# Kernel optimization log

Hardware: AMD Instinct MI355X
Metric: run time of the kernel (lower is better)

Reference implementation:

```python
import jax, jax.numpy as jnp
import numpy as np
import math

B, S, D, H = 2, 2048, 1024, 16
DK = D // H


def setup_inputs() -> dict:
    key = jax.random.key(0)
    ks = jax.random.split(key, 8)
    s = 1.0 / math.sqrt(D)
    inp = {
        "query": jax.random.normal(ks[0], (B, S, D), jnp.float32),
        "key": jax.random.normal(ks[1], (B, S, D), jnp.float32),
        "value": jax.random.normal(ks[2], (B, S, D), jnp.float32),
        # causal mask: (1, 1, S, S), 1 where attention allowed
        "mask": jnp.tril(jnp.ones((S, S), jnp.int32))[None, None, :, :],
        "Wq": jax.random.normal(ks[3], (D, D), jnp.float32) * s,
        "Wk": jax.random.normal(ks[4], (D, D), jnp.float32) * s,
        "Wv": jax.random.normal(ks[5], (D, D), jnp.float32) * s,
        "Wo": jax.random.normal(ks[6], (D, D), jnp.float32) * s,
    }
    return inp


def reference(query, key, value, mask, Wq, Wk, Wv, Wo):
    # nn.Linear(bias=False): y = x @ W.T
    def proj_heads(x, W):
        y = jnp.einsum("bsd,ed->bse", x, W)          # (B,S,D)
        return y.reshape(B, -1, H, DK).transpose(0, 2, 1, 3)  # (B,H,S,DK)

    q = proj_heads(query, Wq)
    k = proj_heads(key, Wk)
    v = proj_heads(value, Wv)

    scale = jnp.asarray(math.sqrt(DK), q.dtype)
    scores = jnp.einsum("bhqd,bhkd->bhqk", q, k) / scale  # (B,H,S,S)
    scores = jnp.where(mask == 0, -jnp.inf, scores)
    attn = jax.nn.softmax(scores, axis=-1)
    # dropout p=0.0 (eval): identity
    out = jnp.einsum("bhqk,bhkd->bhqd", attn, v)          # (B,H,S,DK)
    concat = out.transpose(0, 2, 1, 3).reshape(B, -1, D)  # (B,S,D)
    return jnp.einsum("bsd,ed->bse", concat, Wo)
```

## Files before the change

kernel.cpp:

```cpp
#include <hip/hip_runtime.h>
#include <hip/hip_bf16.h>

#define B_ 2
#define S_ 2048
#define D_ 1024
#define H_ 16
#define DK_ 64

typedef __hip_bfloat16 bf16;
typedef __attribute__((ext_vector_type(8))) short bf16x8;
typedef __attribute__((ext_vector_type(4))) short bf16x4;
typedef __attribute__((ext_vector_type(4))) float f32x4;

#define GLDS16(g, l)                                                     \
    __builtin_amdgcn_global_load_lds(                                    \
        (const __attribute__((address_space(1))) void*)(g),              \
        (__attribute__((address_space(3))) void*)(l), 16, 0, 0)

#define MFMA_K32(a, b, c) __builtin_amdgcn_mfma_f32_16x16x32_bf16(a, b, c, 0, 0, 0)
#define MFMA_K16(a, b, c) __builtin_amdgcn_mfma_f32_16x16x16bf16_1k(a, b, c, 0, 0, 0)
#define EXP2F(x) __builtin_amdgcn_exp2f(x)

__global__ __launch_bounds__(256) void cvt_all(
    const float* __restrict__ q, const float* __restrict__ k, const float* __restrict__ v,
    const float* __restrict__ w0, const float* __restrict__ w1,
    const float* __restrict__ w2, const float* __restrict__ w3,
    bf16* __restrict__ oq, bf16* __restrict__ ok, bf16* __restrict__ ov,
    bf16* __restrict__ o0, bf16* __restrict__ o1, bf16* __restrict__ o2,
    bf16* __restrict__ o3) {
    int bid = blockIdx.x;
    const float* src; bf16* dst; int base;
    if      (bid < 2048) { src = q;  dst = oq; base = bid; }
    else if (bid < 4096) { src = k;  dst = ok; base = bid - 2048; }
    else if (bid < 6144) { src = v;  dst = ov; base = bid - 4096; }
    else if (bid < 6656) { src = w0; dst = o0; base = bid - 6144; }
    else if (bid < 7168) { src = w1; dst = o1; base = bid - 6656; }
    else if (bid < 7680) { src = w2; dst = o2; base = bid - 7168; }
    else                 { src = w3; dst = o3; base = bid - 7680; }
    int i = (base * 256 + threadIdx.x) * 8;
    float4 a = *(const float4*)(src + i);
    float4 b = *(const float4*)(src + i + 4);
    __align__(16) bf16 o[8];
    o[0] = __float2bfloat16(a.x); o[1] = __float2bfloat16(a.y);
    o[2] = __float2bfloat16(a.z); o[3] = __float2bfloat16(a.w);
    o[4] = __float2bfloat16(b.x); o[5] = __float2bfloat16(b.y);
    o[6] = __float2bfloat16(b.z); o[7] = __float2bfloat16(b.w);
    *(bf16x8*)(dst + i) = *(const bf16x8*)o;
}

__device__ __forceinline__ void proj_loop32(const bf16* __restrict__ X,
                                            const bf16* __restrict__ W,
                                            int m0, int n0, bf16* As, bf16* Bs,
                                            f32x4 (&acc)[4][4]) {
    const int K = D_;
    const int tid = threadIdx.x;
    const int lane = tid & 63, wave = tid >> 6;
    const int lm = lane & 15, quad = lane >> 4;
    const int wr = wave >> 1, wc = wave & 1;

    auto stage = [&](int t, int bf) {
        int k0 = t * 32;
        bf16* Ab = As + bf * (128 * 32);
        bf16* Bb = Bs + bf * (128 * 32);
#pragma unroll
        for (int i = 0; i < 2; ++i) {
            int s = i * 256 + tid;
            int row = s >> 2, c = (s & 3) ^ (row & 3);
            GLDS16(X + (size_t)(m0 + row) * K + k0 + c * 8, Ab + s * 8);
        }
#pragma unroll
        for (int i = 0; i < 2; ++i) {
            int s = i * 256 + tid;
            int row = s >> 2, c = (s & 3) ^ (row & 3);
            GLDS16(W + (size_t)(n0 + row) * K + k0 + c * 8, Bb + s * 8);
        }
    };

    stage(0, 0);
    for (int t = 0; t < K / 32; ++t) {
        __syncthreads();
        if (t + 1 < K / 32) stage(t + 1, (t + 1) & 1);
        const bf16* Ab = As + (t & 1) * (128 * 32);
        const bf16* Bb = Bs + (t & 1) * (128 * 32);
        bf16x8 aF[4], bF[4];
#pragma unroll
        for (int mt = 0; mt < 4; ++mt) {
            int row = wr * 64 + mt * 16 + lm;
            aF[mt] = *(const bf16x8*)(Ab + row * 32 + ((quad ^ (row & 3)) * 8));
        }
#pragma unroll
        for (int nt = 0; nt < 4; ++nt) {
            int row = wc * 64 + nt * 16 + lm;
            bF[nt] = *(const bf16x8*)(Bb + row * 32 + ((quad ^ (row & 3)) * 8));
        }
#pragma unroll
        for (int mt = 0; mt < 4; ++mt)
#pragma unroll
            for (int nt = 0; nt < 4; ++nt)
                acc[mt][nt] = MFMA_K32(aF[mt], bF[nt], acc[mt][nt]);
    }
}

__global__ __launch_bounds__(256) void proj_qkv(
    const bf16* __restrict__ qx, const bf16* __restrict__ kx, const bf16* __restrict__ vx,
    const bf16* __restrict__ wq, const bf16* __restrict__ wk, const bf16* __restrict__ wv,
    bf16* __restrict__ qb, bf16* __restrict__ kb, bf16* __restrict__ vtb) {
    __shared__ __align__(16) bf16 As[2 * 128 * 32];
    __shared__ __align__(16) bf16 Bs[2 * 128 * 32];
    const int L = (int)blockIdx.x;
    const int tile = (L & 7) * 96 + (L >> 3);
    const int z = tile >> 8;
    const int rem = tile & 255;
    const int n0 = (rem & 7) * 128;
    const int m0 = (rem >> 3) * 128;
    const bf16* X = (z == 0) ? qx : (z == 1) ? kx : vx;
    const bf16* W = (z == 0) ? wq : (z == 1) ? wk : wv;
    f32x4 acc[4][4] = {};
    proj_loop32(X, W, m0, n0, As, Bs, acc);

    const int lane = threadIdx.x & 63, wave = threadIdx.x >> 6;
    const int lm = lane & 15, quad = lane >> 4;
    const int wr = wave >> 1, wc = wave & 1;
#pragma unroll
    for (int mt = 0; mt < 4; ++mt) {
        int mbase = m0 + wr * 64 + mt * 16 + quad * 4;
#pragma unroll
        for (int nt = 0; nt < 4; ++nt) {
            int n = n0 + wc * 64 + nt * 16 + lm;
            if (z == 2) {
                int b = mbase >> 11, s = mbase & (S_ - 1);
                unsigned short u[4];
#pragma unroll
                for (int r = 0; r < 4; ++r) {
                    bf16 hv = __float2bfloat16(acc[mt][nt][r]);
                    u[r] = *(unsigned short*)&hv;
                }
                ushort4 pk = {u[0], u[1], u[2], u[3]};
                *(ushort4*)(vtb + ((size_t)(b * 1024 + n) * S_ + s)) = pk;
            } else {
                bf16* Y = z ? kb : qb;
#pragma unroll
                for (int r = 0; r < 4; ++r)
                    Y[(size_t)(mbase + r) * D_ + n] = __float2bfloat16(acc[mt][nt][r]);
            }
        }
    }
}

__global__ __launch_bounds__(256) void proj_o(const bf16* __restrict__ X,
                                              const bf16* __restrict__ W,
                                              float* __restrict__ Y) {
    __shared__ __align__(16) bf16 As[2 * 64 * 32];
    __shared__ __align__(16) bf16 Bs[2 * 128 * 32];
    const int L = (int)blockIdx.x;
    const int tile = (L & 7) * 64 + (L >> 3);
    const int n0 = (tile & 7) * 128;
    const int m0 = (tile >> 3) * 64;

    const int K = D_;
    const int tid = threadIdx.x;
    const int lane = tid & 63, wave = tid >> 6;
    const int lm = lane & 15, quad = lane >> 4;
    const int wr = wave >> 1, wc = wave & 1;

    f32x4 acc[2][4] = {};

    auto stage = [&](int t, int bf) {
        int k0 = t * 32;
        bf16* Ab = As + bf * (64 * 32);
        bf16* Bb = Bs + bf * (128 * 32);
        {
            int s = tid;
            int row = s >> 2, c = (s & 3) ^ (row & 3);
            GLDS16(X + (size_t)(m0 + row) * K + k0 + c * 8, Ab + s * 8);
        }
#pragma unroll
        for (int i = 0; i < 2; ++i) {
            int s = i * 256 + tid;
            int row = s >> 2, c = (s & 3) ^ (row & 3);
            GLDS16(W + (size_t)(n0 + row) * K + k0 + c * 8, Bb + s * 8);
        }
    };

    stage(0, 0);
    for (int t = 0; t < K / 32; ++t) {
        __syncthreads();
        if (t + 1 < K / 32) stage(t + 1, (t + 1) & 1);
        const bf16* Ab = As + (t & 1) * (64 * 32);
        const bf16* Bb = Bs + (t & 1) * (128 * 32);
        bf16x8 aF[2], bF[4];
#pragma unroll
        for (int mt = 0; mt < 2; ++mt) {
            int row = wr * 32 + mt * 16 + lm;
            aF[mt] = *(const bf16x8*)(Ab + row * 32 + ((quad ^ (row & 3)) * 8));
        }
#pragma unroll
        for (int nt = 0; nt < 4; ++nt) {
            int row = wc * 64 + nt * 16 + lm;
            bF[nt] = *(const bf16x8*)(Bb + row * 32 + ((quad ^ (row & 3)) * 8));
        }
#pragma unroll
        for (int mt = 0; mt < 2; ++mt)
#pragma unroll
            for (int nt = 0; nt < 4; ++nt)
                acc[mt][nt] = MFMA_K32(aF[mt], bF[nt], acc[mt][nt]);
    }

#pragma unroll
    for (int mt = 0; mt < 2; ++mt) {
        int mbase = m0 + wr * 32 + mt * 16 + quad * 4;
#pragma unroll
        for (int nt = 0; nt < 4; ++nt) {
            int n = n0 + wc * 64 + nt * 16 + lm;
#pragma unroll
            for (int r = 0; r < 4; ++r)
                Y[(size_t)(mbase + r) * D_ + n] = acc[mt][nt][r];
        }
    }
}

__global__ __launch_bounds__(512) void attn_kernel(const bf16* __restrict__ Q,
                                                   const bf16* __restrict__ Kb,
                                                   const bf16* __restrict__ VT,
                                                   bf16* __restrict__ O) {
    __shared__ __align__(16) bf16 kt[2][128 * 64];
    __shared__ __align__(16) bf16 vt[2][64 * 128];

    const int tid = threadIdx.x;
    const int lane = tid & 63, wave = tid >> 6;
    const int lm = lane & 15, quad = lane >> 4;
    const int f = (int)blockIdx.x;
    const int cls = f & 7;
    const int t = f >> 3;
    const int p = t >> 2;
    const int combo = cls + 8 * (t & 3);
    const int b = combo >> 4, h = combo & 15;
    const int qiA = p, qiB = 15 - p;
    const int q0A = qiA * 128 + wave * 16;
    const int q0B = qiB * 128 + wave * 16;

    const size_t bhoff = (size_t)b * S_ * D_ + (size_t)h * DK_;
    const bf16* vtb = VT + ((size_t)b * 1024 + h * DK_) * S_;

    const bf16* qpA = Q + bhoff + (size_t)(q0A + lm) * D_ + quad * 8;
    bf16x8 aqA0 = *(const bf16x8*)(qpA);
    bf16x8 aqA1 = *(const bf16x8*)(qpA + 32);
    const bf16* qpB = Q + bhoff + (size_t)(q0B + lm) * D_ + quad * 8;
    bf16x8 aqB0 = *(const bf16x8*)(qpB);
    bf16x8 aqB1 = *(const bf16x8*)(qpB + 32);

    f32x4 oaccA[4] = {}, oaccB[4] = {};
    float lsumA = 0.f, lsumB = 0.f;
    const float cexp = 0.125f * 1.44269504f;

    auto stage = [&](int i, int bf) {
        int j0s = i * 128;
#pragma unroll
        for (int ii = 0; ii < 2; ++ii) {
            int s = ii * 512 + tid;
            int j = s >> 3, c = (s & 7) ^ (j & 7);
            GLDS16(Kb + bhoff + (size_t)(j0s + j) * D_ + c * 8, kt[bf] + s * 8);
        }
#pragma unroll
        for (int ii = 0; ii < 2; ++ii) {
            int s = ii * 512 + tid;
            int d = s >> 4, c = (s & 15) ^ (d & 15);
            GLDS16(vtb + (size_t)d * S_ + j0s + c * 8, vt[bf] + s * 8);
        }
    };

    auto chunk = [&](const bf16* ktb, const bf16* vtl, int st, bool mk,
                     bf16x8 aq0, bf16x8 aq1, f32x4 (&oacc)[4], float& lsum) {
        int j = st * 16 + lm;
        bf16x8 bk0 = *(const bf16x8*)(ktb + (((j << 3) | (quad ^ (j & 7))) * 8));
        bf16x8 bk1 = *(const bf16x8*)(ktb + (((j << 3) | ((4 + quad) ^ (j & 7))) * 8));
        f32x4 z = {};
        z = MFMA_K32(bk0, aq0, z);
        z = MFMA_K32(bk1, aq1, z);
        bf16x4 pa;
        float rs = 0.f;
#pragma unroll
        for (int r = 0; r < 4; ++r) {
            float pv = EXP2F(z[r] * cexp);
            if (mk && (quad * 4 + r > lm)) pv = 0.f;
            rs += pv;
            bf16 hv = __float2bfloat16(pv);
            pa[r] = *(short*)&hv;
        }
        lsum += rs;
#pragma unroll
        for (int dt = 0; dt < 4; ++dt) {
            int d = dt * 16 + lm;
            int cl = st * 2 + (quad >> 1);
            bf16x4 bv = *(const bf16x4*)(vtl + d * 128 +
                                         ((cl ^ (d & 15)) * 8 + (quad & 1) * 4));
            oacc[dt] = MFMA_K16(pa, bv, oacc[dt]);
        }
    };

    const int nt = qiB + 1;
    stage(0, 0);

    for (int i = 0; i < nt; ++i) {
        __syncthreads();
        if (i + 1 < nt) stage(i + 1, (i + 1) & 1);
        const bf16* ktb = kt[i & 1];
        const bf16* vtl = vt[i & 1];

        if (i < qiB) {
#pragma unroll
            for (int st = 0; st < 8; ++st)
                chunk(ktb, vtl, st, false, aqB0, aqB1, oaccB, lsumB);
        } else {
            for (int st = 0; st < wave; ++st)
                chunk(ktb, vtl, st, false, aqB0, aqB1, oaccB, lsumB);
            chunk(ktb, vtl, wave, true, aqB0, aqB1, oaccB, lsumB);
        }

        if (i < qiA) {
#pragma unroll
            for (int st = 0; st < 8; ++st)
                chunk(ktb, vtl, st, false, aqA0, aqA1, oaccA, lsumA);
        } else if (i == qiA) {
            for (int st = 0; st < wave; ++st)
                chunk(ktb, vtl, st, false, aqA0, aqA1, oaccA, lsumA);
            chunk(ktb, vtl, wave, true, aqA0, aqA1, oaccA, lsumA);
        }
    }

    auto finish = [&](float lsum, f32x4 (&oacc)[4], int q0) {
        float l = lsum;
        l += __shfl_xor(l, 16, 64);
        l += __shfl_xor(l, 32, 64);
#pragma unroll
        for (int r = 0; r < 4; ++r) {
            float inv = 1.f / __shfl(l, quad * 4 + r, 64);
            int qrow = q0 + quad * 4 + r;
#pragma unroll
            for (int dt = 0; dt < 4; ++dt) {
                int d = dt * 16 + lm;
                O[bhoff + (size_t)qrow * D_ + d] = __float2bfloat16(oacc[dt][r] * inv);
            }
        }
    };
    finish(lsumA, oaccA, q0A);
    finish(lsumB, oaccB, q0B);
}

extern "C" void kernel_launch(void* const* d_in, const int* in_sizes, int n_in,
                              void* d_out, int out_size, void* d_ws, size_t ws_size,
                              hipStream_t stream) {
    const float* q_in = (const float*)d_in[0];
    const float* k_in = (const float*)d_in[1];
    const float* v_in = (const float*)d_in[2];
    const float* Wq_f = (const float*)d_in[4];
    const float* Wk_f = (const float*)d_in[5];
    const float* Wv_f = (const float*)d_in[6];
    const float* Wo_f = (const float*)d_in[7];
    float* out = (float*)d_out;

    const size_t NEL = (size_t)B_ * S_ * D_;
    const size_t WEL = (size_t)D_ * D_;
    bf16* p = (bf16*)d_ws;
    bf16* qx = p;  p += NEL;
    bf16* kx = p;  p += NEL;
    bf16* vx = p;  p += NEL;
    bf16* wq = p;  p += WEL;
    bf16* wk = p;  p += WEL;
    bf16* wv = p;  p += WEL;
    bf16* wo = p;  p += WEL;
    bf16* qb = p;  p += NEL;
    bf16* kb = p;  p += NEL;
    bf16* vtb = p; p += NEL;
    bf16* cb = p;  p += NEL;

    cvt_all<<<8192, 256, 0, stream>>>(q_in, k_in, v_in, Wq_f, Wk_f, Wv_f, Wo_f,
                                      qx, kx, vx, wq, wk, wv, wo);

    proj_qkv<<<dim3(768), 256, 0, stream>>>(qx, kx, vx, wq, wk, wv, qb, kb, vtb);

    attn_kernel<<<dim3(256), 512, 0, stream>>>(qb, kb, vtb, cb);

    proj_o<<<dim3(512), 256, 0, stream>>>(cb, wo, out);
}
```

Baseline: 223.9 us.

## Split attention key tiles across two wave groups with LDS reduction

The attention kernel now runs 1024 threads per block. Two groups of 8 waves each take half of the 128-key tile's sub-chunks for the same query rows, and the partial outputs and row sums are merged through shared memory at the end. K and V fragments are now loaded once per sub-chunk and shared between the two query tiles (A and B) rather than reloaded for each. The aim is more waves in flight per CU to hide latency, since only 256 blocks are launched. The cost is extra barriers and an LDS reduction, higher register pressure from the launch_bounds hint, and an unused gproj variable.

```diff
diff --git a/kernel.cpp b/kernel.cpp
--- a/kernel.cpp
+++ b/kernel.cpp
@@ -219,15 +219,17 @@
     }
 }
 
-__global__ __launch_bounds__(512) void attn_kernel(const bf16* __restrict__ Q,
-                                                   const bf16* __restrict__ Kb,
-                                                   const bf16* __restrict__ VT,
-                                                   bf16* __restrict__ O) {
-    __shared__ __align__(16) bf16 kt[2][128 * 64];
-    __shared__ __align__(16) bf16 vt[2][64 * 128];
+__global__ __launch_bounds__(1024, 4) void attn_kernel(const bf16* __restrict__ Q,
+                                                       const bf16* __restrict__ Kb,
+                                                       const bf16* __restrict__ VT,
+                                                       bf16* __restrict__ O) {
+    __shared__ __align__(16) bf16 smem[4 * 128 * 64];
+    bf16* ktb0 = smem;
+    bf16* vtb0 = smem + 2 * 128 * 64;
 
     const int tid = threadIdx.x;
     const int lane = tid & 63, wave = tid >> 6;
+    const int ws = wave & 7, jh = wave >> 3;
     const int lm = lane & 15, quad = lane >> 4;
     const int f = (int)blockIdx.x;
     const int cls = f & 7;
@@ -236,11 +238,11 @@
     const int combo = cls + 8 * (t & 3);
     const int b = combo >> 4, h = combo & 15;
     const int qiA = p, qiB = 15 - p;
-    const int q0A = qiA * 128 + wave * 16;
-    const int q0B = qiB * 128 + wave * 16;
+    const int q0A = qiA * 128 + ws * 16;
+    const int q0B = qiB * 128 + ws * 16;
 
     const size_t bhoff = (size_t)b * S_ * D_ + (size_t)h * DK_;
-    const bf16* vtb = VT + ((size_t)b * 1024 + h * DK_) * S_;
+    const bf16* vtg = VT + ((size_t)b * 1024 + h * DK_) * S_;
 
     const bf16* qpA = Q + bhoff + (size_t)(q0A + lm) * D_ + quad * 8;
     bf16x8 aqA0 = *(const bf16x8*)(qpA);
@@ -255,25 +257,22 @@
 
     auto stage = [&](int i, int bf) {
         int j0s = i * 128;
-#pragma unroll
-        for (int ii = 0; ii < 2; ++ii) {
-            int s = ii * 512 + tid;
+        {
+            int s = tid;
             int j = s >> 3, c = (s & 7) ^ (j & 7);
-            GLDS16(Kb + bhoff + (size_t)(j0s + j) * D_ + c * 8, kt[bf] + s * 8);
-        }
-#pragma unroll
-        for (int ii = 0; ii < 2; ++ii) {
-            int s = ii * 512 + tid;
+            GLDS16(Kb + bhoff + (size_t)(j0s + j) * D_ + c * 8,
+                   ktb0 + bf * (128 * 64) + s * 8);
+        }
+        {
+            int s = tid;
             int d = s >> 4, c = (s & 15) ^ (d & 15);
-            GLDS16(vtb + (size_t)d * S_ + j0s + c * 8, vt[bf] + s * 8);
+            GLDS16(vtg + (size_t)d * S_ + j0s + c * 8,
+                   vtb0 + bf * (64 * 128) + s * 8);
         }
     };
 
-    auto chunk = [&](const bf16* ktb, const bf16* vtl, int st, bool mk,
-                     bf16x8 aq0, bf16x8 aq1, f32x4 (&oacc)[4], float& lsum) {
-        int j = st * 16 + lm;
-        bf16x8 bk0 = *(const bf16x8*)(ktb + (((j << 3) | (quad ^ (j & 7))) * 8));
-        bf16x8 bk1 = *(const bf16x8*)(ktb + (((j << 3) | ((4 + quad) ^ (j & 7))) * 8));
+    auto dochunk = [&](bf16x8 bk0, bf16x8 bk1, const bf16x4 (&bv)[4], bool mk,
+                       bf16x8 aq0, bf16x8 aq1, f32x4 (&oacc)[4], float& lsum) {
         f32x4 z = {};
         z = MFMA_K32(bk0, aq0, z);
         z = MFMA_K32(bk1, aq1, z);
@@ -289,13 +288,8 @@
         }
         lsum += rs;
 #pragma unroll
-        for (int dt = 0; dt < 4; ++dt) {
-            int d = dt * 16 + lm;
-            int cl = st * 2 + (quad >> 1);
-            bf16x4 bv = *(const bf16x4*)(vtl + d * 128 +
-                                         ((cl ^ (d & 15)) * 8 + (quad & 1) * 4));
-            oacc[dt] = MFMA_K16(pa, bv, oacc[dt]);
-        }
+        for (int dt = 0; dt < 4; ++dt)
+            oacc[dt] = MFMA_K16(pa, bv[dt], oacc[dt]);
     };
 
     const int nt = qiB + 1;
@@ -304,47 +298,73 @@
     for (int i = 0; i < nt; ++i) {
         __syncthreads();
         if (i + 1 < nt) stage(i + 1, (i + 1) & 1);
-        const bf16* ktb = kt[i & 1];
-        const bf16* vtl = vt[i & 1];
-
-        if (i < qiB) {
-#pragma unroll
-            for (int st = 0; st < 8; ++st)
-                chunk(ktb, vtl, st, false, aqB0, aqB1, oaccB, lsumB);
-        } else {
-            for (int st = 0; st < wave; ++st)
-                chunk(ktb, vtl, st, false, aqB0, aqB1, oaccB, lsumB);
-            chunk(ktb, vtl, wave, true, aqB0, aqB1, oaccB, lsumB);
-        }
-
-        if (i < qiA) {
-#pragma unroll
-            for (int st = 0; st < 8; ++st)
-                chunk(ktb, vtl, st, false, aqA0, aqA1, oaccA, lsumA);
-        } else if (i == qiA) {
-            for (int st = 0; st < wave; ++st)
-                chunk(ktb, vtl, st, false, aqA0, aqA1, oaccA, lsumA);
-            chunk(ktb, vtl, wave, true, aqA0, aqA1, oaccA, lsumA);
-        }
-    }
-
-    auto finish = [&](float lsum, f32x4 (&oacc)[4], int q0) {
-        float l = lsum;
-        l += __shfl_xor(l, 16, 64);
-        l += __shfl_xor(l, 32, 64);
-#pragma unroll
-        for (int r = 0; r < 4; ++r) {
-            float inv = 1.f / __shfl(l, quad * 4 + r, 64);
-            int qrow = q0 + quad * 4 + r;
+        const bf16* ktb = ktb0 + (i & 1) * (128 * 64);
+        const bf16* vtl = vtb0 + (i & 1) * (64 * 128);
+
+#pragma unroll
+        for (int stl = 0; stl < 4; ++stl) {
+            int sg = jh * 4 + stl;
+            bool actB = (i < qiB) || (sg <= ws);
+            bool mkB  = (i == qiB) && (sg == ws);
+            bool actA = (i < qiA) || ((i == qiA) && (sg <= ws));
+            bool mkA  = (i == qiA) && (sg == ws);
+            if (!actB && !actA) continue;
+
+            int j = sg * 16 + lm;
+            bf16x8 bk0 = *(const bf16x8*)(ktb + (((j << 3) | (quad ^ (j & 7))) * 8));
+            bf16x8 bk1 = *(const bf16x8*)(ktb + (((j << 3) | ((4 + quad) ^ (j & 7))) * 8));
+            bf16x4 bv[4];
 #pragma unroll
             for (int dt = 0; dt < 4; ++dt) {
                 int d = dt * 16 + lm;
-                O[bhoff + (size_t)qrow * D_ + d] = __float2bfloat16(oacc[dt][r] * inv);
+                int cl = sg * 2 + (quad >> 1);
+                bv[dt] = *(const bf16x4*)(vtl + d * 128 +
+                                          ((cl ^ (d & 15)) * 8 + (quad & 1) * 4));
             }
-        }
+            if (actB) dochunk(bk0, bk1, bv, mkB, aqB0, aqB1, oaccB, lsumB);
+            if (actA) dochunk(bk0, bk1, bv, mkA, aqA0, aqA1, oaccA, lsumA);
+        }
+    }
+
+    __syncthreads();
+    float* red = (float*)smem;
+    const int rbase = (ws * 64 + lane) * 17;
+
+    auto reduce_finish = [&](f32x4 (&oacc)[4], float lsum, int q0) {
+        if (jh == 1) {
+#pragma unroll
+            for (int dt = 0; dt < 4; ++dt)
+#pragma unroll
+                for (int r = 0; r < 4; ++r)
+                    red[rbase + dt * 4 + r] = oacc[dt][r];
+            red[rbase + 16] = lsum;
+        }
+        __syncthreads();
+        if (jh == 0) {
+#pragma unroll
+            for (int dt = 0; dt < 4; ++dt)
+#pragma unroll
+                for (int r = 0; r < 4; ++r)
+                    oacc[dt][r] += red[rbase + dt * 4 + r];
+            float l = lsum + red[rbase + 16];
+            l += __shfl_xor(l, 16, 64);
+            l += __shfl_xor(l, 32, 64);
+#pragma unroll
+            for (int r = 0; r < 4; ++r) {
+                float inv = 1.f / __shfl(l, quad * 4 + r, 64);
+                int qrow = q0 + quad * 4 + r;
+#pragma unroll
+                for (int dt = 0; dt < 4; ++dt) {
+                    int d = dt * 16 + lm;
+                    O[bhoff + (size_t)qrow * D_ + d] =
+                        __float2bfloat16(oacc[dt][r] * inv);
+                }
+            }
+        }
+        __syncthreads();
     };
-    finish(lsumA, oaccA, q0A);
-    finish(lsumB, oaccB, q0B);
+    reduce_finish(oaccB, lsumB, q0B);
+    reduce_finish(oaccA, lsumA, q0A);
 }
 
 extern "C" void kernel_launch(void* const* d_in, const int* in_sizes, int n_in,
@@ -379,7 +399,8 @@
 
     proj_qkv<<<dim3(768), 256, 0, stream>>>(qx, kx, vx, wq, wk, wv, qb, kb, vtb);
 
-    attn_kernel<<<dim3(256), 512, 0, stream>>>(qb, kb, vtb, cb);
-
+    attn_kernel<<<dim3(256), 1024, 0, stream>>>(qb, kb, vtb, cb);
+
+    dim3 gproj(D_ / 128, (B_ * S_) / 128);
     proj_o<<<dim3(512), 256, 0, stream>>>(cb, wo, out);
 }
```

Measured after the change: 211.7 us. 5.5% less time.
